# Kernel optimization log

Measured on AMD Instinct MI355X. Metric: run time of the kernel, lower is better.

## Reference

```python
import jax, jax.numpy as jnp
import numpy as np

B, W, M, HD, RL, RD = 32, 32, 1024, 64, 2, 32
D = RL * HD  # concat of per-layer hidden states


def setup_inputs() -> dict:
    key = jax.random.key(0)
    ks = jax.random.split(key, 16)
    s = 0.1
    r = lambda k, shape: (jax.random.normal(k, shape, jnp.float32) * s)
    return {
        "x_input": jax.random.normal(ks[0], (B, W, M), jnp.float32),
        "major_graph": jax.random.normal(ks[1], (M, M), jnp.float32) * 0.02,
        "H_init": jnp.zeros((RL, M, HD), jnp.float32),
        # GRU layer 0: input size 1 -> hidden HD
        "Wih0": r(ks[2], (3 * HD, 1)),
        "Whh0": r(ks[3], (3 * HD, HD)),
        "bih0": jnp.zeros((3 * HD,), jnp.float32),
        "bhh0": jnp.zeros((3 * HD,), jnp.float32),
        # GRU layer 1: hidden HD -> hidden HD
        "Wih1": r(ks[4], (3 * HD, HD)),
        "Whh1": r(ks[5], (3 * HD, HD)),
        "bih1": jnp.zeros((3 * HD,), jnp.float32),
        "bhh1": jnp.zeros((3 * HD,), jnp.float32),
        # weight-normed Linear(RL*HD -> RD)
        "V": r(ks[6], (RD, D)),
        "g": jnp.ones((RD,), jnp.float32),
        "b_lin": jnp.zeros((RD,), jnp.float32),
        # FinalRowWise layer: per-node weights [M, RD] -> scalar per node
        "W_fr": r(ks[7], (M, RD)),
        "b_fr": jnp.zeros((M,), jnp.float32),
    }


def _gru_cell(x, h, Wih, Whh, bih, bhh):
    # x: [B, M, in], h: [B, M, HD]
    gi = x @ Wih.T + bih
    gh = h @ Whh.T + bhh
    ir, iz, inn = jnp.split(gi, 3, axis=-1)
    hr, hz, hnn = jnp.split(gh, 3, axis=-1)
    rgate = jax.nn.sigmoid(ir + hr)
    zgate = jax.nn.sigmoid(iz + hz)
    n = jnp.tanh(inn + rgate * hnn)
    return (1.0 - zgate) * n + zgate * h


def reference(x_input, major_graph, H_init, Wih0, Whh0, bih0, bhh0,
              Wih1, Whh1, bih1, bhh1, V, g, b_lin, W_fr, b_fr):
    Bn, Wn_, Mn = x_input.shape
    # h0: [RL, B, M, HD] (H_init broadcast over batch)
    h0 = jnp.broadcast_to(H_init[:, None], (H_init.shape[0], Bn, Mn, H_init.shape[-1]))
    # weight_norm (dim=0): per-output-row normalization of V scaled by g
    Wn = g[:, None] * V / jnp.linalg.norm(V, axis=1, keepdims=True)  # [RD, D]
    x_seq = jnp.transpose(x_input, (1, 0, 2))[..., None]  # [W, B, M, 1]

    def step(hn, x_t):
        hn0 = _gru_cell(x_t, hn, Wih0, Whh0, bih0, bhh0)        # [B, M, HD]
        hn1 = _gru_cell(hn0, h0[1], Wih1, Whh1, bih1, bhh1)     # [B, M, HD] (fresh h0 each step, as in source)
        x_p = jnp.concatenate([hn0, hn1], axis=-1)              # [B, M, D]
        # graph-weighted projection along node axis: x_p @ major_graph
        x_g = jax.nn.relu(jnp.einsum('bid,ij->bjd', x_p, major_graph))  # [B, M, D]
        y = jax.nn.sigmoid(x_g @ Wn.T + b_lin)                  # [B, M, RD]
        out = jnp.einsum('bmd,md->bm', y, W_fr) + b_fr          # [B, M]
        return hn1, out

    _, outs = jax.lax.scan(step, h0[0], x_seq)  # [W, B, M]
    return jnp.transpose(outs, (1, 0, 2))       # [B, W, M]
```

## Files before the change

### kernel.cpp

```cpp
#include <hip/hip_runtime.h>
#include <math.h>

#define B_  32
#define W_  32
#define M_  1024
#define HD_ 64
#define RD_ 32
#define D_  128
#define CH_ 16
#define NKT 16

typedef short bf16x8 __attribute__((ext_vector_type(8)));
typedef float f32x4  __attribute__((ext_vector_type(4)));

#define AS1 __attribute__((address_space(1)))
#define AS3 __attribute__((address_space(3)))

__device__ __forceinline__ void gload16(const void* g, void* l) {
    __builtin_amdgcn_global_load_lds((const AS1 void*)g, (AS3 void*)l, 16, 0, 0);
}

__device__ __forceinline__ unsigned short f2b(float f) {
    unsigned int u = __float_as_uint(f);
    u += 0x7fffu + ((u >> 16) & 1u);
    return (unsigned short)(u >> 16);
}
__device__ __forceinline__ float b2f(unsigned short h) {
    return __uint_as_float(((unsigned int)h) << 16);
}
__device__ __forceinline__ float sigf(float x) { return 1.0f / (1.0f + __expf(-x)); }
__device__ __forceinline__ float tanhf_(float x) { return 2.0f / (1.0f + __expf(-2.0f * x)) - 1.0f; }


__global__ __launch_bounds__(256) void gt_kernel(const float* __restrict__ G,
                                                 unsigned short* __restrict__ GTb) {
    __shared__ float T[64][65];
    int i0 = blockIdx.x * 64, j0 = blockIdx.y * 64;
    int tid = threadIdx.x;
    int r = tid >> 4, c4 = (tid & 15) * 4;
    #pragma unroll
    for (int q = 0; q < 4; ++q) {
        float4 v = *(const float4*)&G[(i0 + r + q * 16) * M_ + j0 + c4];
        T[r + q * 16][c4] = v.x; T[r + q * 16][c4 + 1] = v.y;
        T[r + q * 16][c4 + 2] = v.z; T[r + q * 16][c4 + 3] = v.w;
    }
    __syncthreads();
    #pragma unroll
    for (int q = 0; q < 4; ++q) {
        int jr = r + q * 16;
        ushort4 o;
        o.x = f2b(T[c4][jr]); o.y = f2b(T[c4 + 1][jr]);
        o.z = f2b(T[c4 + 2][jr]); o.w = f2b(T[c4 + 3][jr]);
        *(ushort4*)&GTb[(j0 + jr) * M_ + i0 + c4] = o;
    }
}

__global__ __launch_bounds__(192) void gh1ct_kernel(const float* __restrict__ H_init,
                                                    const float* __restrict__ Whh1,
                                                    const float* __restrict__ bhh1,
                                                    float* __restrict__ gh1cT) {
    int m = blockIdx.x, k = threadIdx.x;
    __shared__ float h01[HD_];
    if (k < HD_) h01[k] = H_init[(M_ + m) * HD_ + k];
    __syncthreads();
    float d = 0.f;
    #pragma unroll
    for (int hd = 0; hd < HD_; ++hd) d = fmaf(h01[hd], Whh1[k * HD_ + hd], d);
    gh1cT[k * M_ + m] = d + bhh1[k];
}

__global__ __launch_bounds__(128) void wn_kernel(const float* __restrict__ V,
                                                 const float* __restrict__ g,
                                                 unsigned short* __restrict__ Wnb) {
    int r = blockIdx.x, d = threadIdx.x;
    float v = V[r * D_ + d];
    float s = v * v;
    #pragma unroll
    for (int off = 32; off > 0; off >>= 1) s += __shfl_down(s, off);
    __shared__ float ws[2];
    if ((threadIdx.x & 63) == 0) ws[threadIdx.x >> 6] = s;
    __syncthreads();
    float norm = sqrtf(ws[0] + ws[1]);
    Wnb[r * D_ + d] = f2b(g[r] * v / norm);
}

__global__ __launch_bounds__(256) void castw_kernel(const float* __restrict__ Whh0,
                                                    const float* __restrict__ Wih1,
                                                    unsigned short* __restrict__ Whh0b,
                                                    unsigned short* __restrict__ Wih1b) {
    int i = blockIdx.x * 256 + threadIdx.x;
    Whh0b[i] = f2b(Whh0[i]);
    Wih1b[i] = f2b(Wih1[i]);
}

__global__ __launch_bounds__(256) void inith_kernel(const float* __restrict__ H_init,
                                                    unsigned short* __restrict__ Hb) {
    int e8 = blockIdx.x * 256 + threadIdx.x;
    int base = e8 * 8;
    int src = base & (M_ * HD_ - 1);
    float4 v0 = *(const float4*)&H_init[src];
    float4 v1 = *(const float4*)&H_init[src + 4];
    uint4 u;
    u.x = (unsigned int)f2b(v0.x) | ((unsigned int)f2b(v0.y) << 16);
    u.y = (unsigned int)f2b(v0.z) | ((unsigned int)f2b(v0.w) << 16);
    u.z = (unsigned int)f2b(v1.x) | ((unsigned int)f2b(v1.y) << 16);
    u.w = (unsigned int)f2b(v1.z) | ((unsigned int)f2b(v1.w) << 16);
    *(uint4*)&Hb[base] = u;
}

__global__ __launch_bounds__(256) void gru_chunk_kernel(
    const float* __restrict__ x_input, const float* __restrict__ Wih0,
    const float* __restrict__ bih0, const float* __restrict__ bhh0,
    const unsigned short* __restrict__ Whh0b, const unsigned short* __restrict__ Wih1b,
    const float* __restrict__ bih1, const float* __restrict__ gh1cT,
    const float* __restrict__ H_init, unsigned short* __restrict__ Hb,
    unsigned short* __restrict__ XPT_c, int t0)
{
    __shared__ unsigned short Whh0s[192 * 64];
    __shared__ unsigned short Wih1s[192 * 64];
    __shared__ unsigned short hn0s[64 * 64];
    __shared__ unsigned short hn1s[64 * 64];
    const int tid = threadIdx.x, w = tid >> 6, l = tid & 63;
    const int li = l & 15, lh = l >> 4;
    const int b = blockIdx.x >> 4, mt = blockIdx.x & 15;
    const int m0 = mt * 64;
    const int p0b = b * M_ + m0;
    const int ms = m0 + w * 16;

    for (int i = tid; i < 1536; i += 256) {
        int row = i >> 3, pos = i & 7, sc = pos ^ (row & 7);
        gload16(&Whh0b[row * 64 + sc * 8], (char*)Whh0s + (i & ~63) * 16);
        gload16(&Wih1b[row * 64 + sc * 8], (char*)Wih1s + (i & ~63) * 16);
    }
    {
        int p = w * 16 + (l >> 2);
        #pragma unroll
        for (int q = 0; q < 2; ++q) {
            int cc = (l & 3) * 2 + q;
            uint4 v = *(const uint4*)&Hb[(p0b + p) * HD_ + cc * 8];
            *(uint4*)((char*)hn1s + p * 128 + ((cc ^ (p & 7)) << 4)) = v;
        }
    }

    float wi_[3][4], bi0_[3][4], bh0_[3][4], bi1_[3][4];
    float vrA[4][4], vzA[4][4], vnA[4][4], h01A[4][4];
    #pragma unroll
    for (int fi = 0; fi < 4; ++fi) {
        int ko = li + 16 * fi;
        #pragma unroll
        for (int g3 = 0; g3 < 3; ++g3) {
            wi_[g3][fi]  = Wih0[g3 * 64 + ko];
            bi0_[g3][fi] = bih0[g3 * 64 + ko];
            bh0_[g3][fi] = bhh0[g3 * 64 + ko];
            bi1_[g3][fi] = bih1[g3 * 64 + ko];
        }
        float4 vr = *(const float4*)&gh1cT[(ko) * M_ + ms + lh * 4];
        float4 vz = *(const float4*)&gh1cT[(64 + ko) * M_ + ms + lh * 4];
        float4 vn = *(const float4*)&gh1cT[(128 + ko) * M_ + ms + lh * 4];
        vrA[fi][0] = vr.x; vrA[fi][1] = vr.y; vrA[fi][2] = vr.z; vrA[fi][3] = vr.w;
        vzA[fi][0] = vz.x; vzA[fi][1] = vz.y; vzA[fi][2] = vz.z; vzA[fi][3] = vz.w;
        vnA[fi][0] = vn.x; vnA[fi][1] = vn.y; vnA[fi][2] = vn.z; vnA[fi][3] = vn.w;
        #pragma unroll
        for (int reg = 0; reg < 4; ++reg)
            h01A[fi][reg] = H_init[M_ * HD_ + (ms + lh * 4 + reg) * HD_ + ko];
    }

    __syncthreads();

    float hst[4][4];
    #pragma unroll
    for (int fi = 0; fi < 4; ++fi) {
        int ko = li + 16 * fi;
        #pragma unroll
        for (int reg = 0; reg < 4; ++reg) {
            int ml = w * 16 + lh * 4 + reg;
            hst[fi][reg] = b2f(*(const unsigned short*)((char*)hn1s + ml * 128 +
                               ((((ko >> 3) ^ (ml & 7))) << 4) + (ko & 7) * 2));
        }
    }

    for (int ts = 0; ts < CH_; ++ts) {
        int t = t0 + ts;
        float4 xv = *(const float4*)&x_input[(b * W_ + t) * M_ + ms + lh * 4];
        float x4[4] = {xv.x, xv.y, xv.z, xv.w};

        bf16x8 a0_0, a0_1;
        {
            int row = w * 16 + li;
            a0_0 = *(const bf16x8*)((char*)hn1s + row * 128 + ((lh ^ (row & 7)) << 4));
            a0_1 = *(const bf16x8*)((char*)hn1s + row * 128 + (((4 + lh) ^ (row & 7)) << 4));
        }
        f32x4 acc[12];
        #pragma unroll
        for (int nt = 0; nt < 12; ++nt) acc[nt] = (f32x4){0.f, 0.f, 0.f, 0.f};
        #pragma unroll
        for (int nt = 0; nt < 12; ++nt) {
            int row = nt * 16 + li;
            bf16x8 b0 = *(const bf16x8*)((char*)Whh0s + row * 128 + ((lh ^ (row & 7)) << 4));
            bf16x8 b1 = *(const bf16x8*)((char*)Whh0s + row * 128 + (((4 + lh) ^ (row & 7)) << 4));
            acc[nt] = __builtin_amdgcn_mfma_f32_16x16x32_bf16(a0_0, b0, acc[nt], 0, 0, 0);
            acc[nt] = __builtin_amdgcn_mfma_f32_16x16x32_bf16(a0_1, b1, acc[nt], 0, 0, 0);
        }
        #pragma unroll
        for (int reg = 0; reg < 4; ++reg) {
            int ml = w * 16 + lh * 4 + reg;
            #pragma unroll
            for (int fi = 0; fi < 4; ++fi) {
                int j = li + 16 * fi;
                float hprev = hst[fi][reg];
                float gr = acc[fi][reg]     + bh0_[0][fi];
                float gz = acc[4 + fi][reg] + bh0_[1][fi];
                float gn = acc[8 + fi][reg] + bh0_[2][fi];
                float x = x4[reg];
                float r = sigf(x * wi_[0][fi] + bi0_[0][fi] + gr);
                float z = sigf(x * wi_[1][fi] + bi0_[1][fi] + gz);
                float n = tanhf_(x * wi_[2][fi] + bi0_[2][fi] + r * gn);
                float h0v = (1.f - z) * n + z * hprev;
                *(unsigned short*)((char*)hn0s + ml * 128 +
                    ((((j >> 3) ^ (ml & 7))) << 4) + (j & 7) * 2) = f2b(h0v);
            }
        }

        bf16x8 a1_0, a1_1;
        {
            int row = w * 16 + li;
            a1_0 = *(const bf16x8*)((char*)hn0s + row * 128 + ((lh ^ (row & 7)) << 4));
            a1_1 = *(const bf16x8*)((char*)hn0s + row * 128 + (((4 + lh) ^ (row & 7)) << 4));
        }
        #pragma unroll
        for (int nt = 0; nt < 12; ++nt) acc[nt] = (f32x4){0.f, 0.f, 0.f, 0.f};
        #pragma unroll
        for (int nt = 0; nt < 12; ++nt) {
            int row = nt * 16 + li;
            bf16x8 b0 = *(const bf16x8*)((char*)Wih1s + row * 128 + ((lh ^ (row & 7)) << 4));
            bf16x8 b1 = *(const bf16x8*)((char*)Wih1s + row * 128 + (((4 + lh) ^ (row & 7)) << 4));
            acc[nt] = __builtin_amdgcn_mfma_f32_16x16x32_bf16(a1_0, b0, acc[nt], 0, 0, 0);
            acc[nt] = __builtin_amdgcn_mfma_f32_16x16x32_bf16(a1_1, b1, acc[nt], 0, 0, 0);
        }
        #pragma unroll
        for (int fi = 0; fi < 4; ++fi) {
            int ko = li + 16 * fi;
            #pragma unroll
            for (int reg = 0; reg < 4; ++reg) {
                int ml = w * 16 + lh * 4 + reg;
                float r = sigf(acc[fi][reg]     + bi1_[0][fi] + vrA[fi][reg]);
                float z = sigf(acc[4 + fi][reg] + bi1_[1][fi] + vzA[fi][reg]);
                float n = tanhf_(acc[8 + fi][reg] + bi1_[2][fi] + r * vnA[fi][reg]);
                float h1v = (1.f - z) * n + z * h01A[fi][reg];
                hst[fi][reg] = h1v;
                *(unsigned short*)((char*)hn1s + ml * 128 +
                    ((((ko >> 3) ^ (ml & 7))) << 4) + (ko & 7) * 2) = f2b(h1v);
            }
        }

        {
            unsigned short* XPT = XPT_c + (size_t)ts * (D_ * B_ * M_);
            unsigned int pk[8];
            #pragma unroll
            for (int r2 = 0; r2 < 16; r2 += 2) {
                int ma = w * 16 + r2, mb = ma + 1;
                unsigned int ua = *(const unsigned short*)((char*)hn0s + ma * 128 + (((l >> 3) ^ (ma & 7)) << 4) + (l & 7) * 2);
                unsigned int ub = *(const unsigned short*)((char*)hn0s + mb * 128 + (((l >> 3) ^ (mb & 7)) << 4) + (l & 7) * 2);
                pk[r2 >> 1] = ua | (ub << 16);
            }
            uint4 o0 = {pk[0], pk[1], pk[2], pk[3]};
            uint4 o1 = {pk[4], pk[5], pk[6], pk[7]};
            *(uint4*)&XPT[(b * D_ + l) * M_ + ms]     = o0;
            *(uint4*)&XPT[(b * D_ + l) * M_ + ms + 8] = o1;
            #pragma unroll
            for (int r2 = 0; r2 < 16; r2 += 2) {
                int ma = w * 16 + r2, mb = ma + 1;
                unsigned int ua = *(const unsigned short*)((char*)hn1s + ma * 128 + (((l >> 3) ^ (ma & 7)) << 4) + (l & 7) * 2);
                unsigned int ub = *(const unsigned short*)((char*)hn1s + mb * 128 + (((l >> 3) ^ (mb & 7)) << 4) + (l & 7) * 2);
                pk[r2 >> 1] = ua | (ub << 16);
            }
            uint4 o2 = {pk[0], pk[1], pk[2], pk[3]};
            uint4 o3 = {pk[4], pk[5], pk[6], pk[7]};
            *(uint4*)&XPT[(b * D_ + 64 + l) * M_ + ms]     = o2;
            *(uint4*)&XPT[(b * D_ + 64 + l) * M_ + ms + 8] = o3;
        }
    }

    {
        int p = w * 16 + (l >> 2);
        #pragma unroll
        for (int q = 0; q < 2; ++q) {
            int cc = (l & 3) * 2 + q;
            uint4 v = *(const uint4*)((char*)hn1s + p * 128 + ((cc ^ (p & 7)) << 4));
            *(uint4*)&Hb[(p0b + p) * HD_ + cc * 8] = v;
        }
    }
}

__global__ __launch_bounds__(512, 4) void gemmhead_kernel(
    const unsigned short* __restrict__ GTb, const unsigned short* __restrict__ XPT_c,
    const unsigned short* __restrict__ Wnb, const float* __restrict__ b_lin,
    const float* __restrict__ W_fr, const float* __restrict__ b_fr,
    float* __restrict__ out, int t0)
{
    __shared__ __align__(16) char lds[65536];
    const int tid = threadIdx.x, w = tid >> 6, l = tid & 63;
    const int li = l & 15, lh = l >> 4;
    const int wm = w >> 2, wn = w & 3;
    const int bid = blockIdx.x;
    const int ntile = (bid & 7) + ((bid >> 6) << 3);
    const int j0 = ((bid >> 3) & 7) * 128;
    const unsigned short* Asrc = GTb + (size_t)j0 * M_;
    const unsigned short* Bsrc = XPT_c + (size_t)ntile * 128 * M_;

    f32x4 acc[4][2];
    #pragma unroll
    for (int mi = 0; mi < 4; ++mi)
        #pragma unroll
        for (int ni = 0; ni < 2; ++ni) acc[mi][ni] = (f32x4){0.f, 0.f, 0.f, 0.f};

    #define STAGE(kt, c) { \
        _Pragma("unroll") \
        for (int q = 0; q < 2; ++q) { \
            int i = q * 512 + tid; \
            int row = i >> 3, pos = i & 7, sc = pos ^ (row & 7); \
            gload16(&Asrc[row * M_ + (kt) * 64 + sc * 8], lds + (c) * 32768 + (i & ~63) * 16); \
            gload16(&Bsrc[row * M_ + (kt) * 64 + sc * 8], lds + (c) * 32768 + 16384 + (i & ~63) * 16); \
        } }

    STAGE(0, 0);

    for (int kt = 0; kt < NKT; ++kt) {
        if (kt + 1 < NKT) { STAGE(kt + 1, (kt + 1) & 1);
                            asm volatile("s_waitcnt vmcnt(4)" ::: "memory"); }
        else              { asm volatile("s_waitcnt vmcnt(0)" ::: "memory"); }
        __builtin_amdgcn_s_barrier();
        asm volatile("" ::: "memory");
        const char* Abuf = lds + (kt & 1) * 32768;
        const char* Bbuf = Abuf + 16384;
        bf16x8 af[4][2], bfv[2][2];
        #pragma unroll
        for (int mi = 0; mi < 4; ++mi) {
            int row = wm * 64 + mi * 16 + li;
            #pragma unroll
            for (int kk = 0; kk < 2; ++kk)
                af[mi][kk] = *(const bf16x8*)(Abuf + row * 128 + (((kk * 4 + lh) ^ (row & 7)) << 4));
        }
        #pragma unroll
        for (int ni = 0; ni < 2; ++ni) {
            int row = wn * 32 + ni * 16 + li;
            #pragma unroll
            for (int kk = 0; kk < 2; ++kk)
                bfv[ni][kk] = *(const bf16x8*)(Bbuf + row * 128 + (((kk * 4 + lh) ^ (row & 7)) << 4));
        }
        __builtin_amdgcn_s_setprio(1);
        #pragma unroll
        for (int kk = 0; kk < 2; ++kk)
            #pragma unroll
            for (int mi = 0; mi < 4; ++mi)
                #pragma unroll
                for (int ni = 0; ni < 2; ++ni)
                    acc[mi][ni] = __builtin_amdgcn_mfma_f32_16x16x32_bf16(af[mi][kk], bfv[ni][kk], acc[mi][ni], 0, 0, 0);
        __builtin_amdgcn_s_setprio(0);
        asm volatile("s_waitcnt lgkmcnt(0)" ::: "memory");
        __builtin_amdgcn_s_barrier();
        asm volatile("" ::: "memory");
    }

    __syncthreads();

    #pragma unroll
    for (int mi = 0; mi < 4; ++mi)
        #pragma unroll
        for (int ni = 0; ni < 2; ++ni)
            #pragma unroll
            for (int reg = 0; reg < 4; ++reg) {
                int jl = wm * 64 + mi * 16 + lh * 4 + reg;
                int cl = wn * 32 + ni * 16 + li;
                float v = fmaxf(acc[mi][ni][reg], 0.f);
                int byte = jl * 256 + ((((cl >> 3) ^ (jl & 7))) << 4) + (cl & 7) * 2;
                *(unsigned short*)(lds + byte) = f2b(v);
            }
    __syncthreads();

    const int b = ntile & 31, t = t0 + (ntile >> 5);
    float bl0 = b_lin[li], bl1 = b_lin[16 + li];
    {
        int row = w * 16 + li;
        f32x4 P0 = (f32x4){0.f, 0.f, 0.f, 0.f};
        f32x4 P1 = (f32x4){0.f, 0.f, 0.f, 0.f};
        #pragma unroll
        for (int ks = 0; ks < 4; ++ks) {
            int cp = (ks * 4 + lh) ^ (row & 7);
            bf16x8 xa = *(const bf16x8*)(lds + row * 256 + cp * 16);
            bf16x8 wb0 = *(const bf16x8*)&Wnb[(li) * D_ + ks * 32 + lh * 8];
            bf16x8 wb1 = *(const bf16x8*)&Wnb[(16 + li) * D_ + ks * 32 + lh * 8];
            P0 = __builtin_amdgcn_mfma_f32_16x16x32_bf16(xa, wb0, P0, 0, 0, 0);
            P1 = __builtin_amdgcn_mfma_f32_16x16x32_bf16(xa, wb1, P1, 0, 0, 0);
        }
        float s[4];
        #pragma unroll
        for (int reg = 0; reg < 4; ++reg) {
            int j = j0 + w * 16 + lh * 4 + reg;
            float y0 = sigf(P0[reg] + bl0);
            float y1 = sigf(P1[reg] + bl1);
            s[reg] = y0 * W_fr[j * RD_ + li] + y1 * W_fr[j * RD_ + 16 + li];
        }
        #pragma unroll
        for (int off = 1; off < 16; off <<= 1) {
            #pragma unroll
            for (int reg = 0; reg < 4; ++reg) s[reg] += __shfl_xor(s[reg], off);
        }
        if (li == 0) {
            int jb = j0 + w * 16 + lh * 4;
            float4 o = {s[0] + b_fr[jb], s[1] + b_fr[jb + 1],
                        s[2] + b_fr[jb + 2], s[3] + b_fr[jb + 3]};
            *(float4*)&out[(b * W_ + t) * M_ + jb] = o;
        }
    }
}


extern "C" void kernel_launch(void* const* d_in, const int* in_sizes, int n_in,
                              void* d_out, int out_size, void* d_ws, size_t ws_size,
                              hipStream_t stream) {
    const float* x_input = (const float*)d_in[0];
    const float* G       = (const float*)d_in[1];
    const float* H_init  = (const float*)d_in[2];
    const float* Wih0    = (const float*)d_in[3];
    const float* Whh0    = (const float*)d_in[4];
    const float* bih0    = (const float*)d_in[5];
    const float* bhh0    = (const float*)d_in[6];
    const float* Wih1    = (const float*)d_in[7];
    const float* Whh1    = (const float*)d_in[8];
    const float* bih1    = (const float*)d_in[9];
    const float* bhh1    = (const float*)d_in[10];
    const float* V       = (const float*)d_in[11];
    const float* gvec    = (const float*)d_in[12];
    const float* b_lin   = (const float*)d_in[13];
    const float* W_fr    = (const float*)d_in[14];
    const float* b_fr    = (const float*)d_in[15];
    float* out = (float*)d_out;

    char* ws = (char*)d_ws;
    unsigned short* GTb   = (unsigned short*)(ws);
    unsigned short* XPT_c = (unsigned short*)(ws + (2u   << 20));
    unsigned short* Hb    = (unsigned short*)(ws + (130u << 20));
    float*          gh1cT = (float*)(ws + (134u << 20));
    unsigned short* Wnb   = (unsigned short*)(ws + (135u << 20));
    unsigned short* Whh0b = (unsigned short*)(ws + (135u << 20) + 8192);
    unsigned short* Wih1b = (unsigned short*)(ws + (135u << 20) + 8192 + 24576);

    gt_kernel   <<<dim3(16, 16), 256, 0, stream>>>(G, GTb);
    gh1ct_kernel<<<M_, 192, 0, stream>>>(H_init, Whh1, bhh1, gh1cT);
    wn_kernel   <<<RD_, 128, 0, stream>>>(V, gvec, Wnb);
    castw_kernel<<<48, 256, 0, stream>>>(Whh0, Wih1, Whh0b, Wih1b);
    inith_kernel<<<1024, 256, 0, stream>>>(H_init, Hb);

    for (int c = 0; c < W_ / CH_; ++c) {
        gru_chunk_kernel<<<512, 256, 0, stream>>>(x_input, Wih0, bih0, bhh0, Whh0b,
                                                  Wih1b, bih1, gh1cT, H_init, Hb,
                                                  XPT_c, c * CH_);
        gemmhead_kernel<<<dim3(4096), 512, 0, stream>>>(GTb, XPT_c, Wnb, b_lin,
                                                        W_fr, b_fr, out, c * CH_);
    }
}
```

Measured before the change: 666.1 us.

## Split GRU chunk kernel output columns across two waves per row group

```diff
diff --git a/kernel.cpp b/kernel.cpp
--- a/kernel.cpp
+++ b/kernel.cpp
@@ -108,7 +108,7 @@
     *(uint4*)&Hb[base] = u;
 }
 
-__global__ __launch_bounds__(256) void gru_chunk_kernel(
+__global__ __launch_bounds__(512, 4) void gru_chunk_kernel(
     const float* __restrict__ x_input, const float* __restrict__ Wih0,
     const float* __restrict__ bih0, const float* __restrict__ bhh0,
     const unsigned short* __restrict__ Whh0b, const unsigned short* __restrict__ Wih1b,
@@ -122,31 +122,28 @@
     __shared__ unsigned short hn1s[64 * 64];
     const int tid = threadIdx.x, w = tid >> 6, l = tid & 63;
     const int li = l & 15, lh = l >> 4;
+    const int pg = w >> 1, hf = w & 1;
     const int b = blockIdx.x >> 4, mt = blockIdx.x & 15;
     const int m0 = mt * 64;
     const int p0b = b * M_ + m0;
-    const int ms = m0 + w * 16;
-
-    for (int i = tid; i < 1536; i += 256) {
+    const int ms = m0 + pg * 16;
+
+    for (int i = tid; i < 1536; i += 512) {
         int row = i >> 3, pos = i & 7, sc = pos ^ (row & 7);
         gload16(&Whh0b[row * 64 + sc * 8], (char*)Whh0s + (i & ~63) * 16);
         gload16(&Wih1b[row * 64 + sc * 8], (char*)Wih1s + (i & ~63) * 16);
     }
     {
-        int p = w * 16 + (l >> 2);
-        #pragma unroll
-        for (int q = 0; q < 2; ++q) {
-            int cc = (l & 3) * 2 + q;
-            uint4 v = *(const uint4*)&Hb[(p0b + p) * HD_ + cc * 8];
-            *(uint4*)((char*)hn1s + p * 128 + ((cc ^ (p & 7)) << 4)) = v;
-        }
-    }
-
-    float wi_[3][4], bi0_[3][4], bh0_[3][4], bi1_[3][4];
-    float vrA[4][4], vzA[4][4], vnA[4][4], h01A[4][4];
-    #pragma unroll
-    for (int fi = 0; fi < 4; ++fi) {
-        int ko = li + 16 * fi;
+        int p = tid >> 3, cc = tid & 7;
+        uint4 v = *(const uint4*)&Hb[(p0b + p) * HD_ + cc * 8];
+        *(uint4*)((char*)hn1s + p * 128 + ((cc ^ (p & 7)) << 4)) = v;
+    }
+
+    float wi_[3][2], bi0_[3][2], bh0_[3][2], bi1_[3][2];
+    float vrA[2][4], vzA[2][4], vnA[2][4], h01A[2][4];
+    #pragma unroll
+    for (int fi = 0; fi < 2; ++fi) {
+        int ko = hf * 32 + fi * 16 + li;
         #pragma unroll
         for (int g3 = 0; g3 < 3; ++g3) {
             wi_[g3][fi]  = Wih0[g3 * 64 + ko];
@@ -167,13 +164,13 @@
 
     __syncthreads();
 
-    float hst[4][4];
-    #pragma unroll
-    for (int fi = 0; fi < 4; ++fi) {
-        int ko = li + 16 * fi;
+    float hst[2][4];
+    #pragma unroll
+    for (int fi = 0; fi < 2; ++fi) {
+        int ko = hf * 32 + fi * 16 + li;
         #pragma unroll
         for (int reg = 0; reg < 4; ++reg) {
-            int ml = w * 16 + lh * 4 + reg;
+            int ml = pg * 16 + lh * 4 + reg;
             hst[fi][reg] = b2f(*(const unsigned short*)((char*)hn1s + ml * 128 +
                                ((((ko >> 3) ^ (ml & 7))) << 4) + (ko & 7) * 2));
         }
@@ -183,112 +180,96 @@
         int t = t0 + ts;
         float4 xv = *(const float4*)&x_input[(b * W_ + t) * M_ + ms + lh * 4];
         float x4[4] = {xv.x, xv.y, xv.z, xv.w};
-
-        bf16x8 a0_0, a0_1;
-        {
-            int row = w * 16 + li;
-            a0_0 = *(const bf16x8*)((char*)hn1s + row * 128 + ((lh ^ (row & 7)) << 4));
-            a0_1 = *(const bf16x8*)((char*)hn1s + row * 128 + (((4 + lh) ^ (row & 7)) << 4));
-        }
-        f32x4 acc[12];
-        #pragma unroll
-        for (int nt = 0; nt < 12; ++nt) acc[nt] = (f32x4){0.f, 0.f, 0.f, 0.f};
-        #pragma unroll
-        for (int nt = 0; nt < 12; ++nt) {
-            int row = nt * 16 + li;
-            bf16x8 b0 = *(const bf16x8*)((char*)Whh0s + row * 128 + ((lh ^ (row & 7)) << 4));
-            bf16x8 b1 = *(const bf16x8*)((char*)Whh0s + row * 128 + (((4 + lh) ^ (row & 7)) << 4));
-            acc[nt] = __builtin_amdgcn_mfma_f32_16x16x32_bf16(a0_0, b0, acc[nt], 0, 0, 0);
-            acc[nt] = __builtin_amdgcn_mfma_f32_16x16x32_bf16(a0_1, b1, acc[nt], 0, 0, 0);
-        }
-        #pragma unroll
-        for (int reg = 0; reg < 4; ++reg) {
-            int ml = w * 16 + lh * 4 + reg;
-            #pragma unroll
-            for (int fi = 0; fi < 4; ++fi) {
-                int j = li + 16 * fi;
-                float hprev = hst[fi][reg];
-                float gr = acc[fi][reg]     + bh0_[0][fi];
-                float gz = acc[4 + fi][reg] + bh0_[1][fi];
-                float gn = acc[8 + fi][reg] + bh0_[2][fi];
+        const int rl = pg * 16 + li;
+
+        bf16x8 a0 = *(const bf16x8*)((char*)hn1s + rl * 128 + ((lh ^ (rl & 7)) << 4));
+        bf16x8 a1 = *(const bf16x8*)((char*)hn1s + rl * 128 + (((4 + lh) ^ (rl & 7)) << 4));
+        f32x4 acc[6];
+        #pragma unroll
+        for (int q = 0; q < 6; ++q) acc[q] = (f32x4){0.f, 0.f, 0.f, 0.f};
+        #pragma unroll
+        for (int g3 = 0; g3 < 3; ++g3)
+            #pragma unroll
+            for (int fi = 0; fi < 2; ++fi) {
+                int row = (g3 * 4 + hf * 2 + fi) * 16 + li;
+                bf16x8 b0 = *(const bf16x8*)((char*)Whh0s + row * 128 + ((lh ^ (row & 7)) << 4));
+                bf16x8 b1 = *(const bf16x8*)((char*)Whh0s + row * 128 + (((4 + lh) ^ (row & 7)) << 4));
+                acc[g3 * 2 + fi] = __builtin_amdgcn_mfma_f32_16x16x32_bf16(a0, b0, acc[g3 * 2 + fi], 0, 0, 0);
+                acc[g3 * 2 + fi] = __builtin_amdgcn_mfma_f32_16x16x32_bf16(a1, b1, acc[g3 * 2 + fi], 0, 0, 0);
+            }
+        #pragma unroll
+        for (int fi = 0; fi < 2; ++fi) {
+            int j = hf * 32 + fi * 16 + li;
+            #pragma unroll
+            for (int reg = 0; reg < 4; ++reg) {
+                int ml = pg * 16 + lh * 4 + reg;
                 float x = x4[reg];
-                float r = sigf(x * wi_[0][fi] + bi0_[0][fi] + gr);
-                float z = sigf(x * wi_[1][fi] + bi0_[1][fi] + gz);
-                float n = tanhf_(x * wi_[2][fi] + bi0_[2][fi] + r * gn);
-                float h0v = (1.f - z) * n + z * hprev;
+                float r = sigf(x * wi_[0][fi] + bi0_[0][fi] + acc[fi][reg]     + bh0_[0][fi]);
+                float z = sigf(x * wi_[1][fi] + bi0_[1][fi] + acc[2 + fi][reg] + bh0_[1][fi]);
+                float n = tanhf_(x * wi_[2][fi] + bi0_[2][fi] + r * (acc[4 + fi][reg] + bh0_[2][fi]));
+                float h0v = (1.f - z) * n + z * hst[fi][reg];
                 *(unsigned short*)((char*)hn0s + ml * 128 +
                     ((((j >> 3) ^ (ml & 7))) << 4) + (j & 7) * 2) = f2b(h0v);
             }
         }
-
-        bf16x8 a1_0, a1_1;
-        {
-            int row = w * 16 + li;
-            a1_0 = *(const bf16x8*)((char*)hn0s + row * 128 + ((lh ^ (row & 7)) << 4));
-            a1_1 = *(const bf16x8*)((char*)hn0s + row * 128 + (((4 + lh) ^ (row & 7)) << 4));
-        }
-        #pragma unroll
-        for (int nt = 0; nt < 12; ++nt) acc[nt] = (f32x4){0.f, 0.f, 0.f, 0.f};
-        #pragma unroll
-        for (int nt = 0; nt < 12; ++nt) {
-            int row = nt * 16 + li;
-            bf16x8 b0 = *(const bf16x8*)((char*)Wih1s + row * 128 + ((lh ^ (row & 7)) << 4));
-            bf16x8 b1 = *(const bf16x8*)((char*)Wih1s + row * 128 + (((4 + lh) ^ (row & 7)) << 4));
-            acc[nt] = __builtin_amdgcn_mfma_f32_16x16x32_bf16(a1_0, b0, acc[nt], 0, 0, 0);
-            acc[nt] = __builtin_amdgcn_mfma_f32_16x16x32_bf16(a1_1, b1, acc[nt], 0, 0, 0);
-        }
-        #pragma unroll
-        for (int fi = 0; fi < 4; ++fi) {
-            int ko = li + 16 * fi;
+        __syncthreads();
+
+        a0 = *(const bf16x8*)((char*)hn0s + rl * 128 + ((lh ^ (rl & 7)) << 4));
+        a1 = *(const bf16x8*)((char*)hn0s + rl * 128 + (((4 + lh) ^ (rl & 7)) << 4));
+        #pragma unroll
+        for (int q = 0; q < 6; ++q) acc[q] = (f32x4){0.f, 0.f, 0.f, 0.f};
+        #pragma unroll
+        for (int g3 = 0; g3 < 3; ++g3)
+            #pragma unroll
+            for (int fi = 0; fi < 2; ++fi) {
+                int row = (g3 * 4 + hf * 2 + fi) * 16 + li;
+                bf16x8 b0 = *(const bf16x8*)((char*)Wih1s + row * 128 + ((lh ^ (row & 7)) << 4));
+                bf16x8 b1 = *(const bf16x8*)((char*)Wih1s + row * 128 + (((4 + lh) ^ (row & 7)) << 4));
+                acc[g3 * 2 + fi] = __builtin_amdgcn_mfma_f32_16x16x32_bf16(a0, b0, acc[g3 * 2 + fi], 0, 0, 0);
+                acc[g3 * 2 + fi] = __builtin_amdgcn_mfma_f32_16x16x32_bf16(a1, b1, acc[g3 * 2 + fi], 0, 0, 0);
+            }
+        #pragma unroll
+        for (int fi = 0; fi < 2; ++fi) {
+            int ko = hf * 32 + fi * 16 + li;
             #pragma unroll
             for (int reg = 0; reg < 4; ++reg) {
-                int ml = w * 16 + lh * 4 + reg;
+                int ml = pg * 16 + lh * 4 + reg;
                 float r = sigf(acc[fi][reg]     + bi1_[0][fi] + vrA[fi][reg]);
-                float z = sigf(acc[4 + fi][reg] + bi1_[1][fi] + vzA[fi][reg]);
-                float n = tanhf_(acc[8 + fi][reg] + bi1_[2][fi] + r * vnA[fi][reg]);
+                float z = sigf(acc[2 + fi][reg] + bi1_[1][fi] + vzA[fi][reg]);
+                float n = tanhf_(acc[4 + fi][reg] + bi1_[2][fi] + r * vnA[fi][reg]);
                 float h1v = (1.f - z) * n + z * h01A[fi][reg];
                 hst[fi][reg] = h1v;
                 *(unsigned short*)((char*)hn1s + ml * 128 +
                     ((((ko >> 3) ^ (ml & 7))) << 4) + (ko & 7) * 2) = f2b(h1v);
             }
         }
+        __syncthreads();
 
         {
             unsigned short* XPT = XPT_c + (size_t)ts * (D_ * B_ * M_);
+            int d = tid >> 2, mh = (tid & 3) * 16;
+            const char* src = (d < 64) ? (const char*)hn0s : (const char*)hn1s;
+            int dd = d & 63;
             unsigned int pk[8];
             #pragma unroll
-            for (int r2 = 0; r2 < 16; r2 += 2) {
-                int ma = w * 16 + r2, mb = ma + 1;
-                unsigned int ua = *(const unsigned short*)((char*)hn0s + ma * 128 + (((l >> 3) ^ (ma & 7)) << 4) + (l & 7) * 2);
-                unsigned int ub = *(const unsigned short*)((char*)hn0s + mb * 128 + (((l >> 3) ^ (mb & 7)) << 4) + (l & 7) * 2);
-                pk[r2 >> 1] = ua | (ub << 16);
+            for (int mm = 0; mm < 16; mm += 2) {
+                int ma = mh + mm, mb = mh + mm + 1;
+                unsigned int ua = *(const unsigned short*)(src + ma * 128 + (((dd >> 3) ^ (ma & 7)) << 4) + (dd & 7) * 2);
+                unsigned int ub = *(const unsigned short*)(src + mb * 128 + (((dd >> 3) ^ (mb & 7)) << 4) + (dd & 7) * 2);
+                pk[mm >> 1] = ua | (ub << 16);
             }
             uint4 o0 = {pk[0], pk[1], pk[2], pk[3]};
             uint4 o1 = {pk[4], pk[5], pk[6], pk[7]};
-            *(uint4*)&XPT[(b * D_ + l) * M_ + ms]     = o0;
-            *(uint4*)&XPT[(b * D_ + l) * M_ + ms + 8] = o1;
-            #pragma unroll
-            for (int r2 = 0; r2 < 16; r2 += 2) {
-                int ma = w * 16 + r2, mb = ma + 1;
-                unsigned int ua = *(const unsigned short*)((char*)hn1s + ma * 128 + (((l >> 3) ^ (ma & 7)) << 4) + (l & 7) * 2);
-                unsigned int ub = *(const unsigned short*)((char*)hn1s + mb * 128 + (((l >> 3) ^ (mb & 7)) << 4) + (l & 7) * 2);
-                pk[r2 >> 1] = ua | (ub << 16);
-            }
-            uint4 o2 = {pk[0], pk[1], pk[2], pk[3]};
-            uint4 o3 = {pk[4], pk[5], pk[6], pk[7]};
-            *(uint4*)&XPT[(b * D_ + 64 + l) * M_ + ms]     = o2;
-            *(uint4*)&XPT[(b * D_ + 64 + l) * M_ + ms + 8] = o3;
-        }
+            *(uint4*)&XPT[(b * D_ + d) * M_ + m0 + mh]     = o0;
+            *(uint4*)&XPT[(b * D_ + d) * M_ + m0 + mh + 8] = o1;
+        }
+        __syncthreads();
     }
 
     {
-        int p = w * 16 + (l >> 2);
-        #pragma unroll
-        for (int q = 0; q < 2; ++q) {
-            int cc = (l & 3) * 2 + q;
-            uint4 v = *(const uint4*)((char*)hn1s + p * 128 + ((cc ^ (p & 7)) << 4));
-            *(uint4*)&Hb[(p0b + p) * HD_ + cc * 8] = v;
-        }
+        int p = tid >> 3, cc = tid & 7;
+        uint4 v = *(const uint4*)((char*)hn1s + p * 128 + ((cc ^ (p & 7)) << 4));
+        *(uint4*)&Hb[(p0b + p) * HD_ + cc * 8] = v;
     }
 }
 
@@ -453,7 +434,7 @@
     inith_kernel<<<1024, 256, 0, stream>>>(H_init, Hb);
 
     for (int c = 0; c < W_ / CH_; ++c) {
-        gru_chunk_kernel<<<512, 256, 0, stream>>>(x_input, Wih0, bih0, bhh0, Whh0b,
+        gru_chunk_kernel<<<512, 512, 0, stream>>>(x_input, Wih0, bih0, bhh0, Whh0b,
                                                   Wih1b, bih1, gh1cT, H_init, Hb,
                                                   XPT_c, c * CH_);
         gemmhead_kernel<<<dim3(4096), 512, 0, stream>>>(GTb, XPT_c, Wnb, b_lin,
```

Result: faster. 586.5 us (median of 2 runs) (-12.0%).
